# Kernel optimization log

Hardware: AMD Instinct MI355X
Metric: run time of the kernel (lower is better)

Reference implementation:

```python
import jax, jax.numpy as jnp
from jax import lax
import numpy as np

BITS = 16
KSHAPE = (3, 5, 5)
STRIDE = (1, 1, 1)
PAD = (0, 0, 0)
IMG = (2048, 2048)


def setup_inputs() -> dict:
    key = jax.random.key(0)
    k1, k2 = jax.random.split(key)
    x = jax.random.randint(k1, IMG, 0, 2 ** BITS, dtype=jnp.int32)
    weight = jax.random.uniform(k2, KSHAPE, dtype=jnp.float32)
    bias = jnp.zeros((1,), dtype=jnp.float32)
    return {"x": x, "weight": weight, "bias": bias}


def reference(x, weight, bias):
    pad_d, pad_h, pad_w = PAD
    # spatial zero-padding of the integer image
    xp = jnp.pad(x, ((pad_h, pad_h), (pad_w, pad_w)))
    # bit-plane volume: V[z] = bit z of each pixel. (x << pad_d >> s) % 2
    # equals bit (s - pad_d) of x, and is 0 for s < pad_d, i.e. depth
    # zero-padding by pad_d on both sides of the BITS bit-planes.
    z = jnp.arange(BITS, dtype=jnp.int32)
    V = ((xp[None, :, :] >> z[:, None, None]) & 1).astype(jnp.float32)
    V = jnp.pad(V, ((pad_d, pad_d), (0, 0), (0, 0)))  # [D, Hp, Wp]
    # 3D cross-correlation (lax conv does not flip the kernel)
    Y = lax.conv_general_dilated(
        V[None, None],               # [1,1,D,Hp,Wp]
        weight[None, None],          # [1,1,d,h,w]
        window_strides=STRIDE,
        padding="VALID",
        dimension_numbers=("NCDHW", "OIDHW", "NCDHW"),
    )[0, 0]                          # [D_out, H_out, W_out]
    return Y + bias
```

## Files before the change

kernel.cpp:

```cpp
#include <hip/hip_runtime.h>

#define IMG_W 2048
#define IMG_H 2048
#define OUT_W 2044
#define OUT_H 2044
#define OUT_HW (2044 * 2044)

#define TI 16
#define TJ 64
#define LR (TI + 4)
#define LC (TJ + 4)
#define LSTR 69
#define TRP 17

typedef int v4i __attribute__((ext_vector_type(4)));
typedef float v4f __attribute__((ext_vector_type(4)));

__global__ void quant_frag(const float* __restrict__ w, v4i* __restrict__ wfrag) {
    const int l = threadIdx.x;
    const int m = l & 15, g = l >> 4;
    #pragma unroll
    for (int t = 0; t < 7; ++t) {
        const int p = 4 * t + g;
        unsigned b[4] = {0, 0, 0, 0};
        if (p < 25 && m < 14) {
            const int kh = p / 5, kw = p % 5;
            #pragma unroll
            for (int kd = 0; kd < 3; ++kd) {
                const int e = m + kd;
                const unsigned w7 = (unsigned)(int)rintf(w[(kd * 5 + kh) * 5 + kw] * 127.0f);
                b[e >> 2] |= w7 << (8 * (e & 3));
            }
        }
        v4i va;
        va.x = (int)b[0]; va.y = (int)b[1]; va.z = (int)b[2]; va.w = (int)b[3];
        wfrag[t * 64 + l] = va;
    }
}

__global__ __launch_bounds__(256, 4) void conv_mfma(
        const int* __restrict__ x, const v4i* __restrict__ wfrag,
        const float* __restrict__ bias, float* __restrict__ out) {
    __shared__ v4i vt[LR * LSTR];
    __shared__ float trp[4 * 64 * TRP];
    const int tid  = threadIdx.x;
    const int lane = tid & 63;
    const int wv   = tid >> 6;
    const int m16  = lane & 15;
    const int g4   = lane >> 4;
    const int I0 = blockIdx.y * TI;
    const int J0 = blockIdx.x * TJ;

    v4i alo[7];
    #pragma unroll
    for (int t = 0; t < 7; ++t) alo[t] = wfrag[t * 64 + lane];
    const float b0 = bias[0];

    #pragma unroll
    for (int rr = 0; rr < 5; ++rr) {
        const int r  = wv + rr * 4;
        const int gr = min(I0 + r, IMG_H - 1);
        const long rowoff = (long)gr * IMG_W;
        #pragma unroll
        for (int cc = 0; cc < 2; ++cc) {
            const int col = lane + cc * 64;
            if (col < LC) {
                const int gc = min(J0 + col, IMG_W - 1);
                const unsigned v = (unsigned)x[rowoff + gc];
                v4i e;
                e.x = (int)(__umul24( v         & 0xFu, 0x00204081u) & 0x01010101u);
                e.y = (int)(__umul24((v >> 4)   & 0xFu, 0x00204081u) & 0x01010101u);
                e.z = (int)(__umul24((v >> 8)   & 0xFu, 0x00204081u) & 0x01010101u);
                e.w = (int)(__umul24((v >> 12)  & 0xFu, 0x00204081u) & 0x01010101u);
                vt[r * LSTR + col] = e;
            }
        }
    }
    __syncthreads();

    int koff[7];
    #pragma unroll
    for (int t = 0; t < 7; ++t) {
        const int p  = 4 * t + g4;
        const int kh = (p < 25) ? (p / 5) : 0;
        const int kw = (p < 25) ? (p - kh * 5) : 0;
        koff[t] = kh * LSTR + kw;
    }

    const float scale = 1.0f / 127.0f;
    float* twr = trp + wv * (64 * TRP);

    #pragma unroll 1
    for (int il_ = 0; il_ < 4; ++il_) {
        const int il = wv * 4 + il_;

        #pragma unroll
        for (int jg = 0; jg < 4; ++jg) {
            const int rec = il * LSTR + jg * 16 + m16;
            v4i bf[7];
            #pragma unroll
            for (int t = 0; t < 7; ++t) bf[t] = vt[rec + koff[t]];

            v4i ac0 = {0,0,0,0}, ac1 = {0,0,0,0};
            #pragma unroll
            for (int t = 0; t < 6; t += 2) {
                ac0 = __builtin_amdgcn_mfma_i32_16x16x64_i8(alo[t],     bf[t],     ac0, 0, 0, 0);
                ac1 = __builtin_amdgcn_mfma_i32_16x16x64_i8(alo[t + 1], bf[t + 1], ac1, 0, 0, 0);
            }
            ac0 = __builtin_amdgcn_mfma_i32_16x16x64_i8(alo[6], bf[6], ac0, 0, 0, 0);

            v4f o;
            #pragma unroll
            for (int r = 0; r < 4; ++r)
                o[r] = fmaf((float)(ac0[r] + ac1[r]), scale, b0);
            *(v4f*)(twr + (jg * 16 + m16) * TRP + g4 * 4) = o;
        }

        const int i = I0 + il;
        if (i < OUT_H) {
            const int j = J0 + lane;
            const float* tb = twr + lane * TRP;
            float* ob = out + (size_t)i * OUT_W + j;
            const bool jok = j < OUT_W;
            #pragma unroll
            for (int d = 0; d < 14; ++d) {
                if (jok) ob[(size_t)d * OUT_HW] = tb[d];
            }
        }
    }
}

extern "C" void kernel_launch(void* const* d_in, const int* in_sizes, int n_in,
                              void* d_out, int out_size, void* d_ws, size_t ws_size,
                              hipStream_t stream) {
    const int* x      = (const int*)d_in[0];
    const float* w    = (const float*)d_in[1];
    const float* bias = (const float*)d_in[2];
    float* out        = (float*)d_out;
    v4i* wfrag        = (v4i*)d_ws;

    quant_frag<<<1, 64, 0, stream>>>(w, wfrag);
    conv_mfma<<<dim3((OUT_W + TJ - 1) / TJ, (OUT_H + TI - 1) / TI), 256, 0, stream>>>(
        x, wfrag, bias, out);
}
```

Before: 292.6 us.

## Split output rows between MFMA tiles and udot4 dot-product path in one launch

Output rows are partitioned so the top part is handled by the existing int8 MFMA path and the bottom part by a new register-only path that uses packed udot4 instructions on 8-bit weights. Blocks of both kinds are interleaved within one fused grid (7 MFMA blocks and 9 dot blocks per group of 16). The aim is to run matrix-core and vector-ALU work side by side on the same CUs rather than leaving the vector units idle. The dot path quantizes weights at 255 instead of 127, so the two regions have different rounding error, and the fixed partition constants must line up exactly with the image size.

```diff
diff --git a/kernel.cpp b/kernel.cpp
--- a/kernel.cpp
+++ b/kernel.cpp
@@ -12,11 +12,15 @@
 #define LC (TJ + 4)
 #define LSTR 69
 #define TRP 17
+#define MTILES_Y 56
+#define MROWS (MTILES_Y * 16)
+#define TY0 (MROWS / 2)
 
 typedef int v4i __attribute__((ext_vector_type(4)));
 typedef float v4f __attribute__((ext_vector_type(4)));
 
-__global__ void quant_frag(const float* __restrict__ w, v4i* __restrict__ wfrag) {
+__global__ void quant_all(const float* __restrict__ w, v4i* __restrict__ wfrag,
+                          unsigned* __restrict__ wt) {
     const int l = threadIdx.x;
     const int m = l & 15, g = l >> 4;
     #pragma unroll
@@ -36,20 +40,113 @@
         va.x = (int)b[0]; va.y = (int)b[1]; va.z = (int)b[2]; va.w = (int)b[3];
         wfrag[t * 64 + l] = va;
     }
-}
-
-__global__ __launch_bounds__(256, 4) void conv_mfma(
+    if (l < 25) {
+        const int kh = l / 5, kw = l % 5;
+        unsigned w0 = (unsigned)(int)rintf(w[(0 * 5 + kh) * 5 + kw] * 255.0f);
+        unsigned w1 = (unsigned)(int)rintf(w[(1 * 5 + kh) * 5 + kw] * 255.0f);
+        unsigned w2 = (unsigned)(int)rintf(w[(2 * 5 + kh) * 5 + kw] * 255.0f);
+        unsigned W0 = w0 | (w1 << 8) | (w2 << 16);
+        wt[l * 2]     = W0;
+        wt[l * 2 + 1] = W0 << 8;
+    }
+}
+
+template<int HALF>
+__device__ __forceinline__ void body_dot(
+        const int* __restrict__ x, const unsigned* __restrict__ wt,
+        const float* __restrict__ bias, float* __restrict__ out,
+        int bx, int by) {
+    const int lane = threadIdx.x & 63;
+    const int sub  = threadIdx.x >> 6;
+    const int tx = bx * 64 + lane;
+    const int ty = TY0 + by * 4 + sub;
+    if (tx >= 511 || ty >= 1022) return;
+    const int j0 = tx * 4;
+    const int i0 = ty * 2;
+
+    unsigned W0[5][5], W1[5][5];
+    #pragma unroll
+    for (int kh = 0; kh < 5; ++kh)
+        #pragma unroll
+        for (int kw = 0; kw < 5; ++kw) {
+            W0[kh][kw] = wt[(kh * 5 + kw) * 2];
+            W1[kh][kw] = wt[(kh * 5 + kw) * 2 + 1];
+        }
+
+    unsigned acc[2][4][7] = {};
+    const float b0 = bias[0];
+
+    #pragma unroll
+    for (int r = 0; r < 6; ++r) {
+        const int* row = x + (size_t)(i0 + r) * IMG_W + j0;
+        const int4 va = *(const int4*)row;
+        const int4 vb = *(const int4*)(row + 4);
+        const unsigned v[8] = {(unsigned)va.x, (unsigned)va.y, (unsigned)va.z, (unsigned)va.w,
+                               (unsigned)vb.x, (unsigned)vb.y, (unsigned)vb.z, (unsigned)vb.w};
+        #pragma unroll
+        for (int c = 0; c < 8; ++c) {
+            unsigned P[4];
+            #pragma unroll
+            for (int u = 0; u < 4; ++u) {
+                const int t = (HALF ? 3 : 0) + u;
+                P[u] = __umul24((v[c] >> (2 * t)) & 0xFu, 0x00204081u) & 0x01010101u;
+            }
+            #pragma unroll
+            for (int di = 0; di < 2; ++di) {
+                const int kh = r - di;
+                if (kh < 0 || kh > 4) continue;
+                #pragma unroll
+                for (int dj = 0; dj < 4; ++dj) {
+                    const int kw = c - dj;
+                    if (kw < 0 || kw > 4) continue;
+                    const unsigned w0 = W0[kh][kw];
+                    const unsigned w1 = W1[kh][kw];
+                    if (HALF == 0) {
+                        #pragma unroll
+                        for (int u = 0; u < 4; ++u)
+                            acc[di][dj][2 * u] = __builtin_amdgcn_udot4(P[u], w0, acc[di][dj][2 * u], false);
+                        #pragma unroll
+                        for (int u = 0; u < 3; ++u)
+                            acc[di][dj][2 * u + 1] = __builtin_amdgcn_udot4(P[u], w1, acc[di][dj][2 * u + 1], false);
+                    } else {
+                        #pragma unroll
+                        for (int u = 0; u < 4; ++u)
+                            acc[di][dj][2 * u] = __builtin_amdgcn_udot4(P[u], w1, acc[di][dj][2 * u], false);
+                        #pragma unroll
+                        for (int u = 1; u < 4; ++u)
+                            acc[di][dj][2 * u - 1] = __builtin_amdgcn_udot4(P[u], w0, acc[di][dj][2 * u - 1], false);
+                    }
+                }
+            }
+        }
+    }
+
+    const float scale = 1.0f / 255.0f;
+    #pragma unroll
+    for (int di = 0; di < 2; ++di) {
+        const int i = i0 + di;
+        #pragma unroll
+        for (int ld = 0; ld < 7; ++ld) {
+            const int d = (HALF ? 7 : 0) + ld;
+            float4 o;
+            o.x = fmaf((float)acc[di][0][ld], scale, b0);
+            o.y = fmaf((float)acc[di][1][ld], scale, b0);
+            o.z = fmaf((float)acc[di][2][ld], scale, b0);
+            o.w = fmaf((float)acc[di][3][ld], scale, b0);
+            *(float4*)(out + (size_t)d * OUT_HW + (size_t)i * OUT_W + j0) = o;
+        }
+    }
+}
+
+__device__ __forceinline__ void body_mfma(
         const int* __restrict__ x, const v4i* __restrict__ wfrag,
-        const float* __restrict__ bias, float* __restrict__ out) {
-    __shared__ v4i vt[LR * LSTR];
-    __shared__ float trp[4 * 64 * TRP];
+        const float* __restrict__ bias, float* __restrict__ out,
+        int I0, int J0, v4i* vt, float* trp) {
     const int tid  = threadIdx.x;
     const int lane = tid & 63;
     const int wv   = tid >> 6;
     const int m16  = lane & 15;
     const int g4   = lane >> 4;
-    const int I0 = blockIdx.y * TI;
-    const int J0 = blockIdx.x * TJ;
 
     v4i alo[7];
     #pragma unroll
@@ -130,6 +227,28 @@
     }
 }
 
+__global__ __launch_bounds__(256, 4) void conv_fused(
+        const int* __restrict__ x, const v4i* __restrict__ wfrag,
+        const unsigned* __restrict__ wt, const float* __restrict__ bias,
+        float* __restrict__ out) {
+    __shared__ v4i vt[LR * LSTR];
+    __shared__ float trp[4 * 64 * TRP];
+    const int bid = blockIdx.x;
+    const int pe = bid >> 4;
+    const int sl = bid & 15;
+    if (sl < 7) {
+        const int im = pe * 7 + sl;
+        body_mfma(x, wfrag, bias, out, (im >> 5) * 16, (im & 31) * 64, vt, trp);
+    } else {
+        const int id = pe * 9 + (sl - 7);
+        const int z  = id & 1;
+        const int bx = (id >> 1) & 7;
+        const int by = id >> 4;
+        if (z == 0) body_dot<0>(x, wt, bias, out, bx, by);
+        else        body_dot<1>(x, wt, bias, out, bx, by);
+    }
+}
+
 extern "C" void kernel_launch(void* const* d_in, const int* in_sizes, int n_in,
                               void* d_out, int out_size, void* d_ws, size_t ws_size,
                               hipStream_t stream) {
@@ -138,8 +257,8 @@
     const float* bias = (const float*)d_in[2];
     float* out        = (float*)d_out;
     v4i* wfrag        = (v4i*)d_ws;
-
-    quant_frag<<<1, 64, 0, stream>>>(w, wfrag);
-    conv_mfma<<<dim3((OUT_W + TJ - 1) / TJ, (OUT_H + TI - 1) / TI), 256, 0, stream>>>(
-        x, wfrag, bias, out);
-}
+    unsigned* wt      = (unsigned*)(wfrag + 448);
+
+    quant_all<<<1, 64, 0, stream>>>(w, wfrag, wt);
+    conv_fused<<<dim3(4096), 256, 0, stream>>>(x, wfrag, wt, bias, out);
+}
```

Result: faster. 281.0 us (-4.0%).
